# Kernel tuning notes

Hardware: AMD Instinct MI355X
Metric: run time of the kernel (lower is better)

The kernel has to match this reference:

```python
import jax, jax.numpy as jnp
import numpy as np

EPS = 1e-6
NEG = -1e9
RES_RATIO = 1.0  # res_ratio init arg
MAKE_SYM = True


def _ln(x, g, b):
    m = jnp.mean(x, axis=-1, keepdims=True)
    v = jnp.mean((x - m) ** 2, axis=-1, keepdims=True)
    return (x - m) * jax.lax.rsqrt(v + EPS) * g + b


def _sim(q, k, W1q, W1k, b1, W2, b2):
    # NN(concat([q,k])) with first dense split into query/key halves:
    # relu(q@W1q + k@W1k + b1) @ W2 + b2  -> avoids materializing the 2d concat.
    qa = q @ W1q  # [b,n,sq,h]
    kb = k @ W1k  # [b,n,sk,h]
    h1 = jax.nn.relu(qa[:, :, :, None, :] + kb[:, :, None, :, :] + b1)  # [b,n,sq,sk,h]
    s = jnp.einsum('bnqkh,h->bnqk', h1, W2[:, 0]) + b2[0]
    if MAKE_SYM:
        qb = q @ W1k
        ka = k @ W1q
        h2 = jax.nn.relu(ka[:, :, None, :, :] + qb[:, :, :, None, :] + b1)
        s = s + jnp.einsum('bnqkh,h->bnqk', h2, W2[:, 0]) + b2[0]
    return s


def _attention(v, k, q, mask, Ww, bw, Wd, bd, W1q, W1k, b1, W2, b2):
    q = q @ Ww + bw
    k = k @ Ww + bw
    v = v @ Ww + bw
    logits = _sim(q, k, W1q, W1k, b1, W2, b2)
    if mask is not None:
        logits = logits + mask * NEG
    attn = jax.nn.softmax(logits, axis=-1)
    out = jnp.einsum('bnqk,bnkd->bnqd', attn, v)
    return out @ Wd + bd, attn


def setup_inputs() -> dict:
    key = jax.random.key(0)
    B, N, S, D, DFF, H = 4, 1, 256, 128, 512, 128
    ks = jax.random.split(key, 16)
    s = 0.02
    inp = {
        'x': jax.random.normal(ks[0], (B, N, S, D), jnp.float32),
        'enc_output': jax.random.normal(ks[1], (B, N, S, D), jnp.float32),
        'com_mask': jnp.zeros((B, N, S, S), jnp.float32),
        'dec_mask': jnp.zeros((B, N, S, S), jnp.float32),
        # shared pairwise-score MLP NN: Dense(H, relu) -> Dense(1)
        'W1q': jax.random.normal(ks[2], (D, H), jnp.float32) * s,
        'W1k': jax.random.normal(ks[3], (D, H), jnp.float32) * s,
        'b1': jnp.zeros((H,), jnp.float32),
        'W2': jax.random.normal(ks[4], (H, 1), jnp.float32) * s,
        'b2': jnp.zeros((1,), jnp.float32),
        # mha1 projections
        'Ww1': jax.random.normal(ks[5], (D, D), jnp.float32) * s,
        'bw1': jnp.zeros((D,), jnp.float32),
        'Wd1': jax.random.normal(ks[6], (D, D), jnp.float32) * s,
        'bd1': jnp.zeros((D,), jnp.float32),
        # mha2 projections
        'Ww2': jax.random.normal(ks[7], (D, D), jnp.float32) * s,
        'bw2': jnp.zeros((D,), jnp.float32),
        'Wd2': jax.random.normal(ks[8], (D, D), jnp.float32) * s,
        'bd2': jnp.zeros((D,), jnp.float32),
        # ffn
        'Wf1': jax.random.normal(ks[9], (D, DFF), jnp.float32) * s,
        'bf1': jnp.zeros((DFF,), jnp.float32),
        'Wf2': jax.random.normal(ks[10], (DFF, D), jnp.float32) * s,
        'bf2': jnp.zeros((D,), jnp.float32),
        # layernorms
        'ln1_g': jnp.ones((D,), jnp.float32), 'ln1_b': jnp.zeros((D,), jnp.float32),
        'ln2_g': jnp.ones((D,), jnp.float32), 'ln2_b': jnp.zeros((D,), jnp.float32),
        'ln3_g': jnp.ones((D,), jnp.float32), 'ln3_b': jnp.zeros((D,), jnp.float32),
    }
    return inp


def reference(x, enc_output, com_mask, dec_mask,
              W1q, W1k, b1, W2, b2,
              Ww1, bw1, Wd1, bd1,
              Ww2, bw2, Wd2, bd2,
              Wf1, bf1, Wf2, bf2,
              ln1_g, ln1_b, ln2_g, ln2_b, ln3_g, ln3_b):
    r = RES_RATIO
    # self-attention block (dropout inactive, eval mode)
    attn1, aw1 = _attention(x, x, x, com_mask, Ww1, bw1, Wd1, bd1, W1q, W1k, b1, W2, b2)
    out1 = _ln((2 - r) * attn1 + r * x, ln1_g, ln1_b)
    # cross-attention block
    attn2, aw2 = _attention(enc_output, enc_output, out1, dec_mask, Ww2, bw2, Wd2, bd2, W1q, W1k, b1, W2, b2)
    out2 = _ln((2 - r) * attn2 + r * out1, ln2_g, ln2_b)
    # ffn
    ffn = jax.nn.relu(out2 @ Wf1 + bf1) @ Wf2 + bf2
    out3 = _ln((2 - r) * ffn + r * out2, ln3_g, ln3_b)
    return out3
```

## Files before the change

### kernel.cpp

```cpp
#include <hip/hip_runtime.h>
#include <math.h>


#define LN_EPS 1e-6f
#define NEGV  (-1e9f)

constexpr int B = 4, S = 256, D = 128, H = 128, DFF = 512;
constexpr int R = B * S;
constexpr int LDW = H + 4;

struct P {
    const float *x, *enc, *com_mask, *dec_mask;
    const float *W1q, *W1k, *b1, *W2;
    const float *Ww1, *bw1, *Wd1, *bd1;
    const float *Ww2, *bw2, *Wd2, *bd2;
    const float *Wf1, *bf1, *Wf2, *bf2;
    const float *ln1g, *ln1b, *ln2g, *ln2b, *ln3g, *ln3b;
    float *out;
    float *xw, *qa, *kb, *kv2w, *kb2, *ka2, *qa2, *qb2;
    float *sbuf, *sbuf2, *out1;
};

__device__ __forceinline__ float4 mm8(const float* AshS, const float* W,
                                      const float* bias, int lr, int c4)
{
    const float4* W4 = (const float4*)W;
    float4 acc = bias ? ((const float4*)bias)[c4] : make_float4(0.f, 0.f, 0.f, 0.f);
    #pragma unroll 8
    for (int k = 0; k < 128; ++k) {
        const float a = AshS[lr * 128 + k];
        const float4 w = W4[k * 32 + c4];
        acc.x = fmaf(a, w.x, acc.x); acc.y = fmaf(a, w.y, acc.y);
        acc.z = fmaf(a, w.z, acc.z); acc.w = fmaf(a, w.w, acc.w);
    }
    return acc;
}

__global__ __launch_bounds__(256) void proj3_kernel(P p)
{
    const int g = blockIdx.y, tid = threadIdx.x;
    const int r0 = blockIdx.x * 8;
    const int lr = tid >> 5, c4 = tid & 31;
    __shared__ float Ash[8 * 128];
    __shared__ float Pw[8 * 128];

    const float* A    = g ? p.enc  : p.x;
    const float* Wp   = g ? p.Ww2  : p.Ww1;
    const float* bp   = g ? p.bw2  : p.bw1;
    float*       o_w  = g ? p.kv2w : p.xw;
    const float* Wsec = g ? p.W1k  : p.W1q;
    const float* bsec = g ? nullptr: p.b1;
    float*       o_s  = g ? p.kb2  : p.qa;
    const float* Wthr = g ? p.W1q  : p.W1k;
    float*       o_t  = g ? p.ka2  : p.kb;

    ((float4*)Ash)[tid] = ((const float4*)(A + (size_t)r0 * 128))[tid];
    __syncthreads();
    {
        const float4 w = mm8(Ash, Wp, bp, lr, c4);
        ((float4*)(Pw + lr * 128))[c4] = w;
        ((float4*)o_w)[(size_t)(r0 + lr) * 32 + c4] = w;
    }
    __syncthreads();
    {
        const float4 q = mm8(Pw, Wsec, bsec, lr, c4);
        ((float4*)o_s)[(size_t)(r0 + lr) * 32 + c4] = q;
        const float4 k = mm8(Pw, Wthr, nullptr, lr, c4);
        ((float4*)o_t)[(size_t)(r0 + lr) * 32 + c4] = k;
    }
}

#define PW_STEP_N(AP0, AP1, BP0, BP1, A00, A01, A10, A11)                      \
    {                                                                          \
        const float4 w  = *(const float4*)(W2s + h);                           \
        const float4 a0 = *(const float4*)((AP0) + h);                         \
        const float4 a1 = *(const float4*)((AP1) + h);                         \
        const float4 b0 = *(const float4*)((BP0) + h);                         \
        const float4 b1 = *(const float4*)((BP1) + h);                         \
        A00 = fmaf(fmaxf(a0.x+b0.x,0.f),w.x,A00); A00 = fmaf(fmaxf(a0.y+b0.y,0.f),w.y,A00); \
        A00 = fmaf(fmaxf(a0.z+b0.z,0.f),w.z,A00); A00 = fmaf(fmaxf(a0.w+b0.w,0.f),w.w,A00); \
        A01 = fmaf(fmaxf(a0.x+b1.x,0.f),w.x,A01); A01 = fmaf(fmaxf(a0.y+b1.y,0.f),w.y,A01); \
        A01 = fmaf(fmaxf(a0.z+b1.z,0.f),w.z,A01); A01 = fmaf(fmaxf(a0.w+b1.w,0.f),w.w,A01); \
        A10 = fmaf(fmaxf(a1.x+b0.x,0.f),w.x,A10); A10 = fmaf(fmaxf(a1.y+b0.y,0.f),w.y,A10); \
        A10 = fmaf(fmaxf(a1.z+b0.z,0.f),w.z,A10); A10 = fmaf(fmaxf(a1.w+b0.w,0.f),w.w,A10); \
        A11 = fmaf(fmaxf(a1.x+b1.x,0.f),w.x,A11); A11 = fmaf(fmaxf(a1.y+b1.y,0.f),w.y,A11); \
        A11 = fmaf(fmaxf(a1.z+b1.z,0.f),w.z,A11); A11 = fmaf(fmaxf(a1.w+b1.w,0.f),w.w,A11); \
    }

__global__ __launch_bounds__(256) void pairwise_self_kernel(P p)
{
    __shared__ __align__(16) float As[32 * LDW];
    __shared__ __align__(16) float Bs[32 * LDW];
    __shared__ __align__(16) float W2s[H];
    const int b = blockIdx.z, q0 = blockIdx.y * 32, k0 = blockIdx.x * 32;
    const int tid = threadIdx.x, bS = b * S;
    for (int i = tid; i < 32 * (H / 4); i += 256) {
        const int r = i >> 5, c4 = i & 31;
        ((float4*)(As + r * LDW))[c4] = ((const float4*)(p.qa + (size_t)(bS + q0 + r) * H))[c4];
        ((float4*)(Bs + r * LDW))[c4] = ((const float4*)(p.kb + (size_t)(bS + k0 + r) * H))[c4];
    }
    if (tid < H / 4) ((float4*)W2s)[tid] = ((const float4*)p.W2)[tid];
    __syncthreads();
    const int tx = tid & 15, ty = tid >> 4;
    const float* A0 = As + (2 * ty) * LDW; const float* A1 = A0 + LDW;
    const float* B0 = Bs + (2 * tx) * LDW; const float* B1 = B0 + LDW;
    float acc00 = 0.f, acc01 = 0.f, acc10 = 0.f, acc11 = 0.f;
    #pragma unroll 4
    for (int h = 0; h < H; h += 4)
        PW_STEP_N(A0, A1, B0, B1, acc00, acc01, acc10, acc11);
    const size_t base = (size_t)(bS + q0 + 2 * ty) * S + (k0 + 2 * tx);
    *(float2*)(p.sbuf + base)     = make_float2(acc00, acc01);
    *(float2*)(p.sbuf + base + S) = make_float2(acc10, acc11);
}

__global__ __launch_bounds__(256) void pairwise_cross2_kernel(P p)
{
    __shared__ __align__(16) float As1[32 * LDW];
    __shared__ __align__(16) float Bs1[32 * LDW];
    __shared__ __align__(16) float As2[32 * LDW];
    __shared__ __align__(16) float Bs2[32 * LDW];
    __shared__ __align__(16) float W2s[H];
    const int b = blockIdx.z, q0 = blockIdx.y * 32, k0 = blockIdx.x * 32;
    const int tid = threadIdx.x, bS = b * S;

    for (int i = tid; i < 32 * (H / 4); i += 256) {
        const int r = i >> 5, c4 = i & 31;
        ((float4*)(As1 + r * LDW))[c4] = ((const float4*)(p.qa2 + (size_t)(bS + q0 + r) * H))[c4];
        ((float4*)(Bs1 + r * LDW))[c4] = ((const float4*)(p.kb2 + (size_t)(bS + k0 + r) * H))[c4];
        ((float4*)(As2 + r * LDW))[c4] = ((const float4*)(p.qb2 + (size_t)(bS + q0 + r) * H))[c4];
        ((float4*)(Bs2 + r * LDW))[c4] = ((const float4*)(p.ka2 + (size_t)(bS + k0 + r) * H))[c4];
    }
    if (tid < H / 4) ((float4*)W2s)[tid] = ((const float4*)p.W2)[tid];
    __syncthreads();

    const int tx = tid & 15, ty = tid >> 4;
    const float* A0 = As1 + (2 * ty) * LDW; const float* A1 = A0 + LDW;
    const float* B0 = Bs1 + (2 * tx) * LDW; const float* B1 = B0 + LDW;
    const float* C0 = As2 + (2 * ty) * LDW; const float* C1 = C0 + LDW;
    const float* D0 = Bs2 + (2 * tx) * LDW; const float* D1 = D0 + LDW;
    float a00 = 0.f, a01 = 0.f, a10 = 0.f, a11 = 0.f;
    float b00 = 0.f, b01 = 0.f, b10 = 0.f, b11 = 0.f;
    #pragma unroll 4
    for (int h = 0; h < H; h += 4) {
        PW_STEP_N(A0, A1, B0, B1, a00, a01, a10, a11);
        PW_STEP_N(C0, C1, D0, D1, b00, b01, b10, b11);
    }
    const size_t base = (size_t)(bS + q0 + 2 * ty) * S + (k0 + 2 * tx);
    *(float2*)(p.sbuf2 + base)     = make_float2(a00 + b00, a01 + b01);
    *(float2*)(p.sbuf2 + base + S) = make_float2(a10 + b10, a11 + b11);
}

template<bool SYM, bool QPROJ, bool FFN>
__global__ __launch_bounds__(256) void attn_tail_kernel(P p)
{
    __shared__ __align__(16) float smem[FFN ? 8704 : 4096];
    float* rowS = smem;
    float* s8   = smem + 512;
    float* avp  = smem + 1536;
    float* aoS  = smem + 2560;
    float* pp   = smem + 3072;

    const float* Sin  = SYM ? p.sbuf : p.sbuf2;
    const float* mask = SYM ? p.com_mask : p.dec_mask;
    const float* V    = SYM ? p.xw : p.kv2w;
    const float* Wd   = SYM ? p.Wd1 : p.Wd2;
    const float* bd   = SYM ? p.bd1 : p.bd2;
    const float* res  = SYM ? p.x : p.out1;
    const float* lg   = SYM ? p.ln1g : p.ln2g;
    const float* lb   = SYM ? p.ln1b : p.ln2b;

    const int tid = threadIdx.x;
    const int r0 = blockIdx.x * 4, b = r0 >> 8, bS = b * S;

    for (int i = tid; i < 4 * 256; i += 256) {
        const int r = i >> 8, k = i & 255;
        const int row = r0 + r, q = row & 255;
        float l = Sin[(size_t)row * S + k];
        if (SYM) l += Sin[(size_t)(bS + k) * S + q];
        l += mask[(size_t)row * S + k] * NEGV;
        s8[i] = l;
    }
    __syncthreads();

    {
        const int g = tid >> 6, c = tid & 63;
        float* rowp = s8 + g * 256;
        float m = -INFINITY;
        #pragma unroll
        for (int k = c; k < 256; k += 64) m = fmaxf(m, rowp[k]);
        for (int o = 32; o; o >>= 1) m = fmaxf(m, __shfl_xor(m, o, 64));
        float s = 0.f;
        #pragma unroll
        for (int k = c; k < 256; k += 64) { const float e = __expf(rowp[k] - m); rowp[k] = e; s += e; }
        for (int o = 32; o; o >>= 1) s += __shfl_xor(s, o, 64);
        const float rinv = 1.f / s;
        #pragma unroll
        for (int k = c; k < 256; k += 64) rowp[k] *= rinv;
    }
    __syncthreads();

    {
        const int r = tid >> 6, t = tid & 63, c4 = t & 31, kh = t >> 5;
        const float4* V4 = (const float4*)(V + (size_t)bS * D);
        const float* sp = s8 + r * 256 + kh * 128;
        float4 acc = make_float4(0.f, 0.f, 0.f, 0.f);
        #pragma unroll 8
        for (int k = 0; k < 128; ++k) {
            const float a = sp[k];
            const float4 v = V4[(kh * 128 + k) * 32 + c4];
            acc.x = fmaf(a, v.x, acc.x); acc.y = fmaf(a, v.y, acc.y);
            acc.z = fmaf(a, v.z, acc.z); acc.w = fmaf(a, v.w, acc.w);
        }
        ((float4*)avp)[(r * 2 + kh) * 32 + c4] = acc;
    }
    __syncthreads();
    if (tid < 128) {
        const int r = tid >> 5, c4 = tid & 31;
        const float4 a = ((const float4*)avp)[(r * 2 + 0) * 32 + c4];
        const float4 bq = ((const float4*)avp)[(r * 2 + 1) * 32 + c4];
        ((float4*)aoS)[r * 32 + c4] = make_float4(a.x + bq.x, a.y + bq.y, a.z + bq.z, a.w + bq.w);
    }
    __syncthreads();

    {
        const int kh = tid >> 7, unit = tid & 127, r = unit >> 5, c4 = unit & 31;
        const float4* W4 = (const float4*)Wd;
        const float* ap = aoS + r * 128 + kh * 64;
        float4 acc = make_float4(0.f, 0.f, 0.f, 0.f);
        #pragma unroll 8
        for (int k = 0; k < 64; ++k) {
            const float a = ap[k];
            const float4 w = W4[(kh * 64 + k) * 32 + c4];
            acc.x = fmaf(a, w.x, acc.x); acc.y = fmaf(a, w.y, acc.y);
            acc.z = fmaf(a, w.z, acc.z); acc.w = fmaf(a, w.w, acc.w);
        }
        ((float4*)pp)[kh * 128 + unit] = acc;
    }
    __syncthreads();

    if (tid < 128) {
        const int r = tid >> 5, c4 = tid & 31;
        const float4 p0 = ((const float4*)pp)[tid];
        const float4 p1 = ((const float4*)pp)[128 + tid];
        const float4 bv0 = ((const float4*)bd)[c4];
        const float4 r4 = ((const float4*)(res + (size_t)(r0 + r) * 128))[c4];
        const float x0 = p0.x + p1.x + bv0.x + r4.x;
        const float x1 = p0.y + p1.y + bv0.y + r4.y;
        const float x2 = p0.z + p1.z + bv0.z + r4.z;
        const float x3 = p0.w + p1.w + bv0.w + r4.w;
        float s  = x0 + x1 + x2 + x3;
        float s2 = x0 * x0 + x1 * x1 + x2 * x2 + x3 * x3;
        for (int o = 16; o; o >>= 1) { s += __shfl_xor(s, o, 32); s2 += __shfl_xor(s2, o, 32); }
        const float m = s * (1.f / 128), var = s2 * (1.f / 128) - m * m;
        const float rs = rsqrtf(var + LN_EPS);
        const float4 gv = ((const float4*)lg)[c4], bv = ((const float4*)lb)[c4];
        float4 o4;
        o4.x = (x0 - m) * rs * gv.x + bv.x; o4.y = (x1 - m) * rs * gv.y + bv.y;
        o4.z = (x2 - m) * rs * gv.z + bv.z; o4.w = (x3 - m) * rs * gv.w + bv.w;
        ((float4*)rowS)[r * 32 + c4] = o4;
        if (SYM) ((float4*)p.out1)[(size_t)(r0 + r) * 32 + c4] = o4;
    }
    __syncthreads();

    if (QPROJ) {
        float* qpp  = s8;
        float* q2wS = avp;
        {
            const int kh = tid >> 7, unit = tid & 127, r = unit >> 5, c4 = unit & 31;
            const float4* W4 = (const float4*)p.Ww2;
            const float* ap = rowS + r * 128 + kh * 64;
            float4 acc = make_float4(0.f, 0.f, 0.f, 0.f);
            #pragma unroll 8
            for (int k = 0; k < 64; ++k) {
                const float a = ap[k];
                const float4 w = W4[(kh * 64 + k) * 32 + c4];
                acc.x = fmaf(a, w.x, acc.x); acc.y = fmaf(a, w.y, acc.y);
                acc.z = fmaf(a, w.z, acc.z); acc.w = fmaf(a, w.w, acc.w);
            }
            ((float4*)qpp)[kh * 128 + unit] = acc;
        }
        __syncthreads();
        if (tid < 128) {
            const int c4 = tid & 31;
            const float4 p0 = ((const float4*)qpp)[tid];
            const float4 p1 = ((const float4*)qpp)[128 + tid];
            const float4 bw = ((const float4*)p.bw2)[c4];
            ((float4*)q2wS)[tid] = make_float4(p0.x + p1.x + bw.x, p0.y + p1.y + bw.y,
                                               p0.z + p1.z + bw.z, p0.w + p1.w + bw.w);
        }
        __syncthreads();
        {
            const int which = tid >> 7, unit = tid & 127, r = unit >> 5, c4 = unit & 31;
            const float4* W4 = (const float4*)(which ? p.W1k : p.W1q);
            float* oq = which ? p.qb2 : p.qa2;
            const float* ap = q2wS + r * 128;
            float4 acc = ((const float4*)p.b1)[c4];
            #pragma unroll 8
            for (int k = 0; k < 128; ++k) {
                const float a = ap[k];
                const float4 w = W4[k * 32 + c4];
                acc.x = fmaf(a, w.x, acc.x); acc.y = fmaf(a, w.y, acc.y);
                acc.z = fmaf(a, w.z, acc.z); acc.w = fmaf(a, w.w, acc.w);
            }
            ((float4*)oq)[(size_t)(r0 + r) * 32 + c4] = acc;
        }
    }

    if (FFN) {
        float* hidP = smem + 512;
        float* part = smem + 4608;
        {
            const int c = tid & 127, kh = tid >> 7;
            const float4* Wf1_4 = (const float4*)p.Wf1;
            float4 a0 = make_float4(0.f,0.f,0.f,0.f), a1 = a0, a2 = a0, a3 = a0;
            const int kbase = kh * 64;
            #pragma unroll 8
            for (int k = 0; k < 64; ++k) {
                const int kk = kbase + k;
                const float4 w = Wf1_4[kk * 128 + c];
                const float s0 = rowS[kk],       s1 = rowS[128 + kk];
                const float s2 = rowS[256 + kk], s3 = rowS[384 + kk];
                a0.x=fmaf(s0,w.x,a0.x); a0.y=fmaf(s0,w.y,a0.y); a0.z=fmaf(s0,w.z,a0.z); a0.w=fmaf(s0,w.w,a0.w);
                a1.x=fmaf(s1,w.x,a1.x); a1.y=fmaf(s1,w.y,a1.y); a1.z=fmaf(s1,w.z,a1.z); a1.w=fmaf(s1,w.w,a1.w);
                a2.x=fmaf(s2,w.x,a2.x); a2.y=fmaf(s2,w.y,a2.y); a2.z=fmaf(s2,w.z,a2.z); a2.w=fmaf(s2,w.w,a2.w);
                a3.x=fmaf(s3,w.x,a3.x); a3.y=fmaf(s3,w.y,a3.y); a3.z=fmaf(s3,w.z,a3.z); a3.w=fmaf(s3,w.w,a3.w);
            }
            float4* h4 = (float4*)hidP;
            const int base = kh * 512;
            h4[base + 0*128 + c] = a0; h4[base + 1*128 + c] = a1;
            h4[base + 2*128 + c] = a2; h4[base + 3*128 + c] = a3;
        }
        __syncthreads();
        for (int i = tid; i < 2048; i += 256) {
            hidP[i] = fmaxf(hidP[i] + hidP[2048 + i] + p.bf1[i & 511], 0.f);
        }
        __syncthreads();
        {
            const int c4f = tid & 31, kg = tid >> 5;
            const float4* Wf2_4 = (const float4*)p.Wf2;
            float4 a0 = make_float4(0.f,0.f,0.f,0.f), a1 = a0, a2 = a0, a3 = a0;
            const int kbase = kg * 64;
            const float* h0 = hidP + 0 * 512 + kbase;
            const float* h1 = hidP + 1 * 512 + kbase;
            const float* h2 = hidP + 2 * 512 + kbase;
            const float* h3 = hidP + 3 * 512 + kbase;
            #pragma unroll 8
            for (int k = 0; k < 64; ++k) {
                const float4 w = Wf2_4[(kbase + k) * 32 + c4f];
                const float s0 = h0[k], s1 = h1[k], s2 = h2[k], s3 = h3[k];
                a0.x=fmaf(s0,w.x,a0.x); a0.y=fmaf(s0,w.y,a0.y); a0.z=fmaf(s0,w.z,a0.z); a0.w=fmaf(s0,w.w,a0.w);
                a1.x=fmaf(s1,w.x,a1.x); a1.y=fmaf(s1,w.y,a1.y); a1.z=fmaf(s1,w.z,a1.z); a1.w=fmaf(s1,w.w,a1.w);
                a2.x=fmaf(s2,w.x,a2.x); a2.y=fmaf(s2,w.y,a2.y); a2.z=fmaf(s2,w.z,a2.z); a2.w=fmaf(s2,w.w,a2.w);
                a3.x=fmaf(s3,w.x,a3.x); a3.y=fmaf(s3,w.y,a3.y); a3.z=fmaf(s3,w.z,a3.z); a3.w=fmaf(s3,w.w,a3.w);
            }
            float4* p4 = (float4*)part;
            p4[kg * 128 + 0 * 32 + c4f] = a0; p4[kg * 128 + 1 * 32 + c4f] = a1;
            p4[kg * 128 + 2 * 32 + c4f] = a2; p4[kg * 128 + 3 * 32 + c4f] = a3;
        }
        __syncthreads();
        if (tid < 128) {
            const int r = tid >> 5, c4 = tid & 31;
            const float4* p4 = (const float4*)part;
            float4 sum = ((const float4*)p.bf2)[c4];
            #pragma unroll
            for (int kg = 0; kg < 8; ++kg) {
                const float4 v = p4[kg * 128 + r * 32 + c4];
                sum.x += v.x; sum.y += v.y; sum.z += v.z; sum.w += v.w;
            }
            const float4 r4 = ((const float4*)rowS)[r * 32 + c4];
            const float x0 = sum.x + r4.x, x1 = sum.y + r4.y;
            const float x2 = sum.z + r4.z, x3 = sum.w + r4.w;
            float s  = x0 + x1 + x2 + x3;
            float s2 = x0 * x0 + x1 * x1 + x2 * x2 + x3 * x3;
            for (int o = 16; o; o >>= 1) { s += __shfl_xor(s, o, 32); s2 += __shfl_xor(s2, o, 32); }
            const float m = s * (1.f / 128), var = s2 * (1.f / 128) - m * m;
            const float rs = rsqrtf(var + LN_EPS);
            const float4 gv = ((const float4*)p.ln3g)[c4], bv = ((const float4*)p.ln3b)[c4];
            float4 o4;
            o4.x = (x0 - m) * rs * gv.x + bv.x; o4.y = (x1 - m) * rs * gv.y + bv.y;
            o4.z = (x2 - m) * rs * gv.z + bv.z; o4.w = (x3 - m) * rs * gv.w + bv.w;
            ((float4*)p.out)[(size_t)(r0 + r) * 32 + c4] = o4;
        }
    }
}

extern "C" void kernel_launch(void* const* d_in, const int* in_sizes, int n_in,
                              void* d_out, int out_size, void* d_ws, size_t ws_size,
                              hipStream_t stream) {
    (void)in_sizes; (void)n_in; (void)out_size; (void)ws_size;
    P p;
    p.x        = (const float*)d_in[0];
    p.enc      = (const float*)d_in[1];
    p.com_mask = (const float*)d_in[2];
    p.dec_mask = (const float*)d_in[3];
    p.W1q = (const float*)d_in[4];
    p.W1k = (const float*)d_in[5];
    p.b1  = (const float*)d_in[6];
    p.W2  = (const float*)d_in[7];
    p.Ww1 = (const float*)d_in[9];
    p.bw1 = (const float*)d_in[10];
    p.Wd1 = (const float*)d_in[11];
    p.bd1 = (const float*)d_in[12];
    p.Ww2 = (const float*)d_in[13];
    p.bw2 = (const float*)d_in[14];
    p.Wd2 = (const float*)d_in[15];
    p.bd2 = (const float*)d_in[16];
    p.Wf1 = (const float*)d_in[17];
    p.bf1 = (const float*)d_in[18];
    p.Wf2 = (const float*)d_in[19];
    p.bf2 = (const float*)d_in[20];
    p.ln1g = (const float*)d_in[21];
    p.ln1b = (const float*)d_in[22];
    p.ln2g = (const float*)d_in[23];
    p.ln2b = (const float*)d_in[24];
    p.ln3g = (const float*)d_in[25];
    p.ln3b = (const float*)d_in[26];
    p.out  = (float*)d_out;

    float* ws = (float*)d_ws;
    const size_t RD  = (size_t)R * D;
    const size_t SSz = (size_t)B * S * S;
    p.xw    = ws;
    p.qa    = p.xw    + RD;
    p.kb    = p.qa    + RD;
    p.kv2w  = p.kb    + RD;
    p.kb2   = p.kv2w  + RD;
    p.ka2   = p.kb2   + RD;
    p.qa2   = p.ka2   + RD;
    p.qb2   = p.qa2   + RD;
    p.sbuf  = p.qb2   + RD;
    p.sbuf2 = p.sbuf  + SSz;
    p.out1  = p.sbuf2 + SSz;

    proj3_kernel<<<dim3(R / 8, 2), 256, 0, stream>>>(p);
    pairwise_self_kernel<<<dim3(8, 8, 4), 256, 0, stream>>>(p);
    attn_tail_kernel<true, true, false><<<R / 4, 256, 0, stream>>>(p);
    pairwise_cross2_kernel<<<dim3(8, 8, 4), 256, 0, stream>>>(p);
    attn_tail_kernel<false, false, true><<<R / 4, 256, 0, stream>>>(p);
}
```

Before: 182.3 us.

## Double block size to 512 threads with split-K partial reductions in all kernels

Every kernel is launched with 512 threads instead of 256. The extra threads split the reduction dimension (K or H) into more chunks, and the partial sums are combined through shared memory. This raises per-block parallelism for a small problem that launches only 256–512 blocks, so latency-bound inner loops get shorter. In exchange it adds shared-memory traffic, extra barriers and a larger LDS footprint, which may lower occupancy, and half the threads sit idle in the softmax and reduction phases.

```diff
diff --git a/kernel.cpp b/kernel.cpp
--- a/kernel.cpp
+++ b/kernel.cpp
@@ -21,28 +21,13 @@
     float *sbuf, *sbuf2, *out1;
 };
 
-__device__ __forceinline__ float4 mm8(const float* AshS, const float* W,
-                                      const float* bias, int lr, int c4)
-{
-    const float4* W4 = (const float4*)W;
-    float4 acc = bias ? ((const float4*)bias)[c4] : make_float4(0.f, 0.f, 0.f, 0.f);
-    #pragma unroll 8
-    for (int k = 0; k < 128; ++k) {
-        const float a = AshS[lr * 128 + k];
-        const float4 w = W4[k * 32 + c4];
-        acc.x = fmaf(a, w.x, acc.x); acc.y = fmaf(a, w.y, acc.y);
-        acc.z = fmaf(a, w.z, acc.z); acc.w = fmaf(a, w.w, acc.w);
-    }
-    return acc;
-}
-
-__global__ __launch_bounds__(256) void proj3_kernel(P p)
+__global__ __launch_bounds__(512) void proj3_kernel(P p)
 {
     const int g = blockIdx.y, tid = threadIdx.x;
     const int r0 = blockIdx.x * 8;
-    const int lr = tid >> 5, c4 = tid & 31;
-    __shared__ float Ash[8 * 128];
-    __shared__ float Pw[8 * 128];
+    __shared__ __align__(16) float Ash[8 * 128];
+    __shared__ __align__(16) float Pw[8 * 128];
+    __shared__ __align__(16) float Pp[2 * 8 * 128];
 
     const float* A    = g ? p.enc  : p.x;
     const float* Wp   = g ? p.Ww2  : p.Ww1;
@@ -54,19 +39,50 @@
     const float* Wthr = g ? p.W1q  : p.W1k;
     float*       o_t  = g ? p.ka2  : p.kb;
 
-    ((float4*)Ash)[tid] = ((const float4*)(A + (size_t)r0 * 128))[tid];
-    __syncthreads();
+    if (tid < 256)
+        ((float4*)Ash)[tid] = ((const float4*)(A + (size_t)r0 * 128))[tid];
+    __syncthreads();
+
     {
-        const float4 w = mm8(Ash, Wp, bp, lr, c4);
-        ((float4*)(Pw + lr * 128))[c4] = w;
+        const int kh = tid >> 8, unit = tid & 255, lr = unit >> 5, c4 = unit & 31;
+        const float4* W4 = (const float4*)Wp;
+        float4 acc = (kh == 0) ? ((const float4*)bp)[c4] : make_float4(0.f, 0.f, 0.f, 0.f);
+        const int k0 = kh * 64;
+        #pragma unroll 8
+        for (int k = 0; k < 64; ++k) {
+            const float a = Ash[lr * 128 + k0 + k];
+            const float4 w = W4[(k0 + k) * 32 + c4];
+            acc.x = fmaf(a, w.x, acc.x); acc.y = fmaf(a, w.y, acc.y);
+            acc.z = fmaf(a, w.z, acc.z); acc.w = fmaf(a, w.w, acc.w);
+        }
+        ((float4*)Pp)[kh * 256 + unit] = acc;
+    }
+    __syncthreads();
+    if (tid < 256) {
+        const int lr = tid >> 5, c4 = tid & 31;
+        const float4 a = ((const float4*)Pp)[tid];
+        const float4 bq = ((const float4*)Pp)[256 + tid];
+        const float4 w = make_float4(a.x + bq.x, a.y + bq.y, a.z + bq.z, a.w + bq.w);
+        ((float4*)Pw)[tid] = w;
         ((float4*)o_w)[(size_t)(r0 + lr) * 32 + c4] = w;
     }
     __syncthreads();
+
     {
-        const float4 q = mm8(Pw, Wsec, bsec, lr, c4);
-        ((float4*)o_s)[(size_t)(r0 + lr) * 32 + c4] = q;
-        const float4 k = mm8(Pw, Wthr, nullptr, lr, c4);
-        ((float4*)o_t)[(size_t)(r0 + lr) * 32 + c4] = k;
+        const int which = tid >> 8, unit = tid & 255, lr = unit >> 5, c4 = unit & 31;
+        const float* W = which ? Wthr : Wsec;
+        const float* bb = which ? nullptr : bsec;
+        float* o = which ? o_t : o_s;
+        const float4* W4 = (const float4*)W;
+        float4 acc = bb ? ((const float4*)bb)[c4] : make_float4(0.f, 0.f, 0.f, 0.f);
+        #pragma unroll 8
+        for (int k = 0; k < 128; ++k) {
+            const float a = Pw[lr * 128 + k];
+            const float4 w = W4[k * 32 + c4];
+            acc.x = fmaf(a, w.x, acc.x); acc.y = fmaf(a, w.y, acc.y);
+            acc.z = fmaf(a, w.z, acc.z); acc.w = fmaf(a, w.w, acc.w);
+        }
+        ((float4*)o)[(size_t)(r0 + lr) * 32 + c4] = acc;
     }
 }
 
@@ -87,43 +103,54 @@
         A11 = fmaf(fmaxf(a1.z+b1.z,0.f),w.z,A11); A11 = fmaf(fmaxf(a1.w+b1.w,0.f),w.w,A11); \
     }
 
-__global__ __launch_bounds__(256) void pairwise_self_kernel(P p)
+__global__ __launch_bounds__(512) void pairwise_self_kernel(P p)
 {
     __shared__ __align__(16) float As[32 * LDW];
     __shared__ __align__(16) float Bs[32 * LDW];
     __shared__ __align__(16) float W2s[H];
+    __shared__ __align__(16) float Pp[256 * 4];
     const int b = blockIdx.z, q0 = blockIdx.y * 32, k0 = blockIdx.x * 32;
     const int tid = threadIdx.x, bS = b * S;
-    for (int i = tid; i < 32 * (H / 4); i += 256) {
+    for (int i = tid; i < 32 * (H / 4); i += 512) {
         const int r = i >> 5, c4 = i & 31;
         ((float4*)(As + r * LDW))[c4] = ((const float4*)(p.qa + (size_t)(bS + q0 + r) * H))[c4];
         ((float4*)(Bs + r * LDW))[c4] = ((const float4*)(p.kb + (size_t)(bS + k0 + r) * H))[c4];
     }
     if (tid < H / 4) ((float4*)W2s)[tid] = ((const float4*)p.W2)[tid];
     __syncthreads();
-    const int tx = tid & 15, ty = tid >> 4;
+    const int hh = tid >> 8, unit = tid & 255;
+    const int tx = unit & 15, ty = unit >> 4;
     const float* A0 = As + (2 * ty) * LDW; const float* A1 = A0 + LDW;
     const float* B0 = Bs + (2 * tx) * LDW; const float* B1 = B0 + LDW;
     float acc00 = 0.f, acc01 = 0.f, acc10 = 0.f, acc11 = 0.f;
+    const int hbase = hh * 64;
     #pragma unroll 4
-    for (int h = 0; h < H; h += 4)
+    for (int hi = 0; hi < 64; hi += 4) {
+        const int h = hbase + hi;
         PW_STEP_N(A0, A1, B0, B1, acc00, acc01, acc10, acc11);
-    const size_t base = (size_t)(bS + q0 + 2 * ty) * S + (k0 + 2 * tx);
-    *(float2*)(p.sbuf + base)     = make_float2(acc00, acc01);
-    *(float2*)(p.sbuf + base + S) = make_float2(acc10, acc11);
+    }
+    if (hh) ((float4*)Pp)[unit] = make_float4(acc00, acc01, acc10, acc11);
+    __syncthreads();
+    if (!hh) {
+        const float4 o = ((const float4*)Pp)[unit];
+        const size_t base = (size_t)(bS + q0 + 2 * ty) * S + (k0 + 2 * tx);
+        *(float2*)(p.sbuf + base)     = make_float2(acc00 + o.x, acc01 + o.y);
+        *(float2*)(p.sbuf + base + S) = make_float2(acc10 + o.z, acc11 + o.w);
+    }
 }
 
-__global__ __launch_bounds__(256) void pairwise_cross2_kernel(P p)
+__global__ __launch_bounds__(512) void pairwise_cross2_kernel(P p)
 {
     __shared__ __align__(16) float As1[32 * LDW];
     __shared__ __align__(16) float Bs1[32 * LDW];
     __shared__ __align__(16) float As2[32 * LDW];
     __shared__ __align__(16) float Bs2[32 * LDW];
     __shared__ __align__(16) float W2s[H];
+    __shared__ __align__(16) float Pp8[256 * 8];
     const int b = blockIdx.z, q0 = blockIdx.y * 32, k0 = blockIdx.x * 32;
     const int tid = threadIdx.x, bS = b * S;
 
-    for (int i = tid; i < 32 * (H / 4); i += 256) {
+    for (int i = tid; i < 32 * (H / 4); i += 512) {
         const int r = i >> 5, c4 = i & 31;
         ((float4*)(As1 + r * LDW))[c4] = ((const float4*)(p.qa2 + (size_t)(bS + q0 + r) * H))[c4];
         ((float4*)(Bs1 + r * LDW))[c4] = ((const float4*)(p.kb2 + (size_t)(bS + k0 + r) * H))[c4];
@@ -133,32 +160,44 @@
     if (tid < H / 4) ((float4*)W2s)[tid] = ((const float4*)p.W2)[tid];
     __syncthreads();
 
-    const int tx = tid & 15, ty = tid >> 4;
+    const int hh = tid >> 8, unit = tid & 255;
+    const int tx = unit & 15, ty = unit >> 4;
     const float* A0 = As1 + (2 * ty) * LDW; const float* A1 = A0 + LDW;
     const float* B0 = Bs1 + (2 * tx) * LDW; const float* B1 = B0 + LDW;
     const float* C0 = As2 + (2 * ty) * LDW; const float* C1 = C0 + LDW;
     const float* D0 = Bs2 + (2 * tx) * LDW; const float* D1 = D0 + LDW;
     float a00 = 0.f, a01 = 0.f, a10 = 0.f, a11 = 0.f;
     float b00 = 0.f, b01 = 0.f, b10 = 0.f, b11 = 0.f;
+    const int hbase = hh * 64;
     #pragma unroll 4
-    for (int h = 0; h < H; h += 4) {
+    for (int hi = 0; hi < 64; hi += 4) {
+        const int h = hbase + hi;
         PW_STEP_N(A0, A1, B0, B1, a00, a01, a10, a11);
         PW_STEP_N(C0, C1, D0, D1, b00, b01, b10, b11);
     }
-    const size_t base = (size_t)(bS + q0 + 2 * ty) * S + (k0 + 2 * tx);
-    *(float2*)(p.sbuf2 + base)     = make_float2(a00 + b00, a01 + b01);
-    *(float2*)(p.sbuf2 + base + S) = make_float2(a10 + b10, a11 + b11);
+    if (hh) {
+        ((float4*)Pp8)[unit * 2]     = make_float4(a00, a01, a10, a11);
+        ((float4*)Pp8)[unit * 2 + 1] = make_float4(b00, b01, b10, b11);
+    }
+    __syncthreads();
+    if (!hh) {
+        const float4 o1 = ((const float4*)Pp8)[unit * 2];
+        const float4 o2 = ((const float4*)Pp8)[unit * 2 + 1];
+        const size_t base = (size_t)(bS + q0 + 2 * ty) * S + (k0 + 2 * tx);
+        *(float2*)(p.sbuf2 + base)     = make_float2(a00 + b00 + o1.x + o2.x, a01 + b01 + o1.y + o2.y);
+        *(float2*)(p.sbuf2 + base + S) = make_float2(a10 + b10 + o1.z + o2.z, a11 + b11 + o1.w + o2.w);
+    }
 }
 
 template<bool SYM, bool QPROJ, bool FFN>
-__global__ __launch_bounds__(256) void attn_tail_kernel(P p)
+__global__ __launch_bounds__(512) void attn_tail_kernel(P p)
 {
-    __shared__ __align__(16) float smem[FFN ? 8704 : 4096];
+    __shared__ __align__(16) float smem[FFN ? 16896 : 6144];
     float* rowS = smem;
     float* s8   = smem + 512;
     float* avp  = smem + 1536;
-    float* aoS  = smem + 2560;
-    float* pp   = smem + 3072;
+    float* aoS  = smem + 3584;
+    float* pp   = smem + 4096;
 
     const float* Sin  = SYM ? p.sbuf : p.sbuf2;
     const float* mask = SYM ? p.com_mask : p.dec_mask;
@@ -172,7 +211,7 @@
     const int tid = threadIdx.x;
     const int r0 = blockIdx.x * 4, b = r0 >> 8, bS = b * S;
 
-    for (int i = tid; i < 4 * 256; i += 256) {
+    for (int i = tid; i < 4 * 256; i += 512) {
         const int r = i >> 8, k = i & 255;
         const int row = r0 + r, q = row & 255;
         float l = Sin[(size_t)row * S + k];
@@ -184,57 +223,63 @@
 
     {
         const int g = tid >> 6, c = tid & 63;
-        float* rowp = s8 + g * 256;
-        float m = -INFINITY;
-        #pragma unroll
-        for (int k = c; k < 256; k += 64) m = fmaxf(m, rowp[k]);
-        for (int o = 32; o; o >>= 1) m = fmaxf(m, __shfl_xor(m, o, 64));
-        float s = 0.f;
-        #pragma unroll
-        for (int k = c; k < 256; k += 64) { const float e = __expf(rowp[k] - m); rowp[k] = e; s += e; }
-        for (int o = 32; o; o >>= 1) s += __shfl_xor(s, o, 64);
-        const float rinv = 1.f / s;
-        #pragma unroll
-        for (int k = c; k < 256; k += 64) rowp[k] *= rinv;
+        if (g < 4) {
+            float* rowp = s8 + g * 256;
+            float m = -INFINITY;
+            #pragma unroll
+            for (int k = c; k < 256; k += 64) m = fmaxf(m, rowp[k]);
+            for (int o = 32; o; o >>= 1) m = fmaxf(m, __shfl_xor(m, o, 64));
+            float s = 0.f;
+            #pragma unroll
+            for (int k = c; k < 256; k += 64) { const float e = __expf(rowp[k] - m); rowp[k] = e; s += e; }
+            for (int o = 32; o; o >>= 1) s += __shfl_xor(s, o, 64);
+            const float rinv = 1.f / s;
+            #pragma unroll
+            for (int k = c; k < 256; k += 64) rowp[k] *= rinv;
+        }
     }
     __syncthreads();
 
     {
-        const int r = tid >> 6, t = tid & 63, c4 = t & 31, kh = t >> 5;
+        const int r = tid >> 7, t = tid & 127, kq = t >> 5, c4 = t & 31;
         const float4* V4 = (const float4*)(V + (size_t)bS * D);
-        const float* sp = s8 + r * 256 + kh * 128;
-        float4 acc = make_float4(0.f, 0.f, 0.f, 0.f);
-        #pragma unroll 8
-        for (int k = 0; k < 128; ++k) {
-            const float a = sp[k];
-            const float4 v = V4[(kh * 128 + k) * 32 + c4];
-            acc.x = fmaf(a, v.x, acc.x); acc.y = fmaf(a, v.y, acc.y);
-            acc.z = fmaf(a, v.z, acc.z); acc.w = fmaf(a, v.w, acc.w);
-        }
-        ((float4*)avp)[(r * 2 + kh) * 32 + c4] = acc;
-    }
-    __syncthreads();
-    if (tid < 128) {
-        const int r = tid >> 5, c4 = tid & 31;
-        const float4 a = ((const float4*)avp)[(r * 2 + 0) * 32 + c4];
-        const float4 bq = ((const float4*)avp)[(r * 2 + 1) * 32 + c4];
-        ((float4*)aoS)[r * 32 + c4] = make_float4(a.x + bq.x, a.y + bq.y, a.z + bq.z, a.w + bq.w);
-    }
-    __syncthreads();
-
-    {
-        const int kh = tid >> 7, unit = tid & 127, r = unit >> 5, c4 = unit & 31;
-        const float4* W4 = (const float4*)Wd;
-        const float* ap = aoS + r * 128 + kh * 64;
+        const float* sp = s8 + r * 256 + kq * 64;
         float4 acc = make_float4(0.f, 0.f, 0.f, 0.f);
         #pragma unroll 8
         for (int k = 0; k < 64; ++k) {
+            const float a = sp[k];
+            const float4 v = V4[(kq * 64 + k) * 32 + c4];
+            acc.x = fmaf(a, v.x, acc.x); acc.y = fmaf(a, v.y, acc.y);
+            acc.z = fmaf(a, v.z, acc.z); acc.w = fmaf(a, v.w, acc.w);
+        }
+        ((float4*)avp)[(r * 4 + kq) * 32 + c4] = acc;
+    }
+    __syncthreads();
+    if (tid < 128) {
+        const int r = tid >> 5, c4 = tid & 31;
+        float4 s0 = ((const float4*)avp)[(r * 4 + 0) * 32 + c4];
+        const float4 s1 = ((const float4*)avp)[(r * 4 + 1) * 32 + c4];
+        const float4 s2 = ((const float4*)avp)[(r * 4 + 2) * 32 + c4];
+        const float4 s3 = ((const float4*)avp)[(r * 4 + 3) * 32 + c4];
+        s0.x += s1.x + s2.x + s3.x; s0.y += s1.y + s2.y + s3.y;
+        s0.z += s1.z + s2.z + s3.z; s0.w += s1.w + s2.w + s3.w;
+        ((float4*)aoS)[r * 32 + c4] = s0;
+    }
+    __syncthreads();
+
+    {
+        const int kq = tid >> 7, unit = tid & 127, r = unit >> 5, c4 = unit & 31;
+        const float4* W4 = (const float4*)Wd;
+        const float* ap = aoS + r * 128 + kq * 32;
+        float4 acc = make_float4(0.f, 0.f, 0.f, 0.f);
+        #pragma unroll 8
+        for (int k = 0; k < 32; ++k) {
             const float a = ap[k];
-            const float4 w = W4[(kh * 64 + k) * 32 + c4];
+            const float4 w = W4[(kq * 32 + k) * 32 + c4];
             acc.x = fmaf(a, w.x, acc.x); acc.y = fmaf(a, w.y, acc.y);
             acc.z = fmaf(a, w.z, acc.z); acc.w = fmaf(a, w.w, acc.w);
         }
-        ((float4*)pp)[kh * 128 + unit] = acc;
+        ((float4*)pp)[kq * 128 + unit] = acc;
     }
     __syncthreads();
 
@@ -242,12 +287,14 @@
         const int r = tid >> 5, c4 = tid & 31;
         const float4 p0 = ((const float4*)pp)[tid];
         const float4 p1 = ((const float4*)pp)[128 + tid];
+        const float4 p2 = ((const float4*)pp)[256 + tid];
+        const float4 p3 = ((const float4*)pp)[384 + tid];
         const float4 bv0 = ((const float4*)bd)[c4];
         const float4 r4 = ((const float4*)(res + (size_t)(r0 + r) * 128))[c4];
-        const float x0 = p0.x + p1.x + bv0.x + r4.x;
-        const float x1 = p0.y + p1.y + bv0.y + r4.y;
-        const float x2 = p0.z + p1.z + bv0.z + r4.z;
-        const float x3 = p0.w + p1.w + bv0.w + r4.w;
+        const float x0 = p0.x + p1.x + p2.x + p3.x + bv0.x + r4.x;
+        const float x1 = p0.y + p1.y + p2.y + p3.y + bv0.y + r4.y;
+        const float x2 = p0.z + p1.z + p2.z + p3.z + bv0.z + r4.z;
+        const float x3 = p0.w + p1.w + p2.w + p3.w + bv0.w + r4.w;
         float s  = x0 + x1 + x2 + x3;
         float s2 = x0 * x0 + x1 * x1 + x2 * x2 + x3 * x3;
         for (int o = 16; o; o >>= 1) { s += __shfl_xor(s, o, 32); s2 += __shfl_xor(s2, o, 32); }
@@ -263,12 +310,43 @@
     __syncthreads();
 
     if (QPROJ) {
-        float* qpp  = s8;
-        float* q2wS = avp;
+        float* qpp  = smem + 512;
+        float* q2wS = smem + 2560;
+        float* qp2  = smem + 1536;
         {
-            const int kh = tid >> 7, unit = tid & 127, r = unit >> 5, c4 = unit & 31;
+            const int kq = tid >> 7, unit = tid & 127, r = unit >> 5, c4 = unit & 31;
             const float4* W4 = (const float4*)p.Ww2;
-            const float* ap = rowS + r * 128 + kh * 64;
+            const float* ap = rowS + r * 128 + kq * 32;
+            float4 acc = make_float4(0.f, 0.f, 0.f, 0.f);
+            #pragma unroll 8
+            for (int k = 0; k < 32; ++k) {
+                const float a = ap[k];
+                const float4 w = W4[(kq * 32 + k) * 32 + c4];
+                acc.x = fmaf(a, w.x, acc.x); acc.y = fmaf(a, w.y, acc.y);
+                acc.z = fmaf(a, w.z, acc.z); acc.w = fmaf(a, w.w, acc.w);
+            }
+            ((float4*)qpp)[kq * 128 + unit] = acc;
+        }
+        __syncthreads();
+        if (tid < 128) {
+            const int c4 = tid & 31;
+            const float4 p0 = ((const float4*)qpp)[tid];
+            const float4 p1 = ((const float4*)qpp)[128 + tid];
+            const float4 p2 = ((const float4*)qpp)[256 + tid];
+            const float4 p3 = ((const float4*)qpp)[384 + tid];
+            const float4 bw = ((const float4*)p.bw2)[c4];
+            ((float4*)q2wS)[tid] = make_float4(p0.x + p1.x + p2.x + p3.x + bw.x,
+                                               p0.y + p1.y + p2.y + p3.y + bw.y,
+                                               p0.z + p1.z + p2.z + p3.z + bw.z,
+                                               p0.w + p1.w + p2.w + p3.w + bw.w);
+        }
+        __syncthreads();
+        {
+            const int which = tid >> 8, sub = tid & 255;
+            const int kh = sub >> 7, unit2 = sub & 127;
+            const float4* W4 = (const float4*)(which ? p.W1k : p.W1q);
+            const int r = unit2 >> 5, c4 = unit2 & 31;
+            const float* ap = q2wS + r * 128 + kh * 64;
             float4 acc = make_float4(0.f, 0.f, 0.f, 0.f);
             #pragma unroll 8
             for (int k = 0; k < 64; ++k) {
@@ -277,45 +355,32 @@
                 acc.x = fmaf(a, w.x, acc.x); acc.y = fmaf(a, w.y, acc.y);
                 acc.z = fmaf(a, w.z, acc.z); acc.w = fmaf(a, w.w, acc.w);
             }
-            ((float4*)qpp)[kh * 128 + unit] = acc;
+            ((float4*)qp2)[(which * 2 + kh) * 128 + unit2] = acc;
         }
         __syncthreads();
-        if (tid < 128) {
-            const int c4 = tid & 31;
-            const float4 p0 = ((const float4*)qpp)[tid];
-            const float4 p1 = ((const float4*)qpp)[128 + tid];
-            const float4 bw = ((const float4*)p.bw2)[c4];
-            ((float4*)q2wS)[tid] = make_float4(p0.x + p1.x + bw.x, p0.y + p1.y + bw.y,
-                                               p0.z + p1.z + bw.z, p0.w + p1.w + bw.w);
-        }
-        __syncthreads();
-        {
-            const int which = tid >> 7, unit = tid & 127, r = unit >> 5, c4 = unit & 31;
-            const float4* W4 = (const float4*)(which ? p.W1k : p.W1q);
+        if (tid < 256) {
+            const int which = tid >> 7, unit2 = tid & 127;
+            const int r = unit2 >> 5, c4 = unit2 & 31;
+            const float4 p0 = ((const float4*)qp2)[(which * 2 + 0) * 128 + unit2];
+            const float4 p1 = ((const float4*)qp2)[(which * 2 + 1) * 128 + unit2];
+            const float4 b1v = ((const float4*)p.b1)[c4];
             float* oq = which ? p.qb2 : p.qa2;
-            const float* ap = q2wS + r * 128;
-            float4 acc = ((const float4*)p.b1)[c4];
-            #pragma unroll 8
-            for (int k = 0; k < 128; ++k) {
-                const float a = ap[k];
-                const float4 w = W4[k * 32 + c4];
-                acc.x = fmaf(a, w.x, acc.x); acc.y = fmaf(a, w.y, acc.y);
-                acc.z = fmaf(a, w.z, acc.z); acc.w = fmaf(a, w.w, acc.w);
-            }
-            ((float4*)oq)[(size_t)(r0 + r) * 32 + c4] = acc;
+            ((float4*)oq)[(size_t)(r0 + r) * 32 + c4] =
+                make_float4(p0.x + p1.x + b1v.x, p0.y + p1.y + b1v.y,
+                            p0.z + p1.z + b1v.z, p0.w + p1.w + b1v.w);
         }
     }
 
     if (FFN) {
         float* hidP = smem + 512;
-        float* part = smem + 4608;
+        float* part = smem + 8704;
         {
             const int c = tid & 127, kh = tid >> 7;
             const float4* Wf1_4 = (const float4*)p.Wf1;
             float4 a0 = make_float4(0.f,0.f,0.f,0.f), a1 = a0, a2 = a0, a3 = a0;
-            const int kbase = kh * 64;
+            const int kbase = kh * 32;
             #pragma unroll 8
-            for (int k = 0; k < 64; ++k) {
+            for (int k = 0; k < 32; ++k) {
                 const int kk = kbase + k;
                 const float4 w = Wf1_4[kk * 128 + c];
                 const float s0 = rowS[kk],       s1 = rowS[128 + kk];
@@ -331,21 +396,22 @@
             h4[base + 2*128 + c] = a2; h4[base + 3*128 + c] = a3;
         }
         __syncthreads();
-        for (int i = tid; i < 2048; i += 256) {
-            hidP[i] = fmaxf(hidP[i] + hidP[2048 + i] + p.bf1[i & 511], 0.f);
+        for (int i = tid; i < 2048; i += 512) {
+            hidP[i] = fmaxf(hidP[i] + hidP[2048 + i] + hidP[4096 + i] + hidP[6144 + i]
+                            + p.bf1[i & 511], 0.f);
         }
         __syncthreads();
         {
             const int c4f = tid & 31, kg = tid >> 5;
             const float4* Wf2_4 = (const float4*)p.Wf2;
             float4 a0 = make_float4(0.f,0.f,0.f,0.f), a1 = a0, a2 = a0, a3 = a0;
-            const int kbase = kg * 64;
+            const int kbase = kg * 32;
             const float* h0 = hidP + 0 * 512 + kbase;
             const float* h1 = hidP + 1 * 512 + kbase;
             const float* h2 = hidP + 2 * 512 + kbase;
             const float* h3 = hidP + 3 * 512 + kbase;
             #pragma unroll 8
-            for (int k = 0; k < 64; ++k) {
+            for (int k = 0; k < 32; ++k) {
                 const float4 w = Wf2_4[(kbase + k) * 32 + c4f];
                 const float s0 = h0[k], s1 = h1[k], s2 = h2[k], s3 = h3[k];
                 a0.x=fmaf(s0,w.x,a0.x); a0.y=fmaf(s0,w.y,a0.y); a0.z=fmaf(s0,w.z,a0.z); a0.w=fmaf(s0,w.w,a0.w);
@@ -363,7 +429,7 @@
             const float4* p4 = (const float4*)part;
             float4 sum = ((const float4*)p.bf2)[c4];
             #pragma unroll
-            for (int kg = 0; kg < 8; ++kg) {
+            for (int kg = 0; kg < 16; ++kg) {
                 const float4 v = p4[kg * 128 + r * 32 + c4];
                 sum.x += v.x; sum.y += v.y; sum.z += v.z; sum.w += v.w;
             }
@@ -432,9 +498,9 @@
     p.sbuf2 = p.sbuf  + SSz;
     p.out1  = p.sbuf2 + SSz;
 
-    proj3_kernel<<<dim3(R / 8, 2), 256, 0, stream>>>(p);
-    pairwise_self_kernel<<<dim3(8, 8, 4), 256, 0, stream>>>(p);
-    attn_tail_kernel<true, true, false><<<R / 4, 256, 0, stream>>>(p);
-    pairwise_cross2_kernel<<<dim3(8, 8, 4), 256, 0, stream>>>(p);
-    attn_tail_kernel<false, false, true><<<R / 4, 256, 0, stream>>>(p);
+    proj3_kernel<<<dim3(R / 8, 2), 512, 0, stream>>>(p);
+    pairwise_self_kernel<<<dim3(8, 8, 4), 512, 0, stream>>>(p);
+    attn_tail_kernel<true, true, false><<<R / 4, 512, 0, stream>>>(p);
+    pairwise_cross2_kernel<<<dim3(8, 8, 4), 512, 0, stream>>>(p);
+    attn_tail_kernel<false, false, true><<<R / 4, 512, 0, stream>>>(p);
 }
```

Measured after the change: 172.0 us. 5.6% less time.
